# Kernel tuning notes

Measured on AMD Instinct MI355X. Metric: run time of the kernel, lower is better.

Reference implementation:

```python
import jax, jax.numpy as jnp
import numpy as np

HID = 64
N_P = 150000
N_B = 250000
E = 500000
D_NODE = 32
D_EDGE = 16
NEG_ACT = 0.01  # module-level LeakyReLU default slope
NEG_ATT = 0.2   # GATConv attention LeakyReLU slope


def _seg_softmax(logits, seg, n):
    m = jax.ops.segment_max(logits, seg, num_segments=n)
    m = jnp.where(jnp.isfinite(m), m, 0.0)
    e = jnp.exp(logits - m[seg])
    s = jax.ops.segment_sum(e, seg, num_segments=n)
    return e / (s[seg] + 1e-16)


def _gat_edges(h_src, h_dst, he, src, dst, asrc, adst, aedge, bias, n_dst):
    # per-node attention pieces, gathered per edge (heads=1)
    a = (h_src @ asrc)[src] + (h_dst @ adst)[dst] + he @ aedge  # [E]
    alpha = _seg_softmax(jax.nn.leaky_relu(a, NEG_ATT), dst, n_dst)
    out = jax.ops.segment_sum(h_src[src] * alpha[:, None], dst, num_segments=n_dst)
    return out + bias


def _homo_gat(x, ei, ea, W, We, asrc, adst, aedge, bias):
    # PyG GATConv with add_self_loops=True, fill_value='mean' for edge_attr
    n = x.shape[0]
    h = x @ W
    he = ea @ We
    loop = jnp.arange(n)
    src = jnp.concatenate([ei[0], loop])
    dst = jnp.concatenate([ei[1], loop])
    he_full = jnp.concatenate([he, jnp.broadcast_to(he.mean(0), (n, he.shape[1]))])
    return _gat_edges(h, h, he_full, src, dst, asrc, adst, aedge, bias, n)


def _bi_gat(x_src, x_dst, ei, ea, Wsrc, Wdst, We, asrc, adst, aedge, bias):
    # bipartite GATConv, add_self_loops=False
    return _gat_edges(x_src @ Wsrc, x_dst @ Wdst, ea @ We, ei[0], ei[1],
                      asrc, adst, aedge, bias, x_dst.shape[0])


def setup_inputs():
    kit = iter(jax.random.split(jax.random.key(0), 100))
    def rn(shape, s):
        return jax.random.normal(next(kit), shape, jnp.float32) * s
    s_h = 1.0 / np.sqrt(HID)
    inp = {}
    inp["x_p"] = rn((N_P, D_NODE), 1.0)
    inp["x_b"] = rn((N_B, D_NODE), 1.0)
    for r in ("pp", "bb", "bp"):
        inp["ea_" + r] = rn((E, D_EDGE), 1.0)
    inp["W_node_p"] = rn((D_NODE, HID), 1.0 / np.sqrt(D_NODE)); inp["b_node_p"] = jnp.zeros((HID,), jnp.float32)
    inp["W_node_b"] = rn((D_NODE, HID), 1.0 / np.sqrt(D_NODE)); inp["b_node_b"] = jnp.zeros((HID,), jnp.float32)
    for r in ("pp", "bb", "bp"):
        inp["W_edge_" + r] = rn((D_EDGE, HID), 1.0 / np.sqrt(D_EDGE))
        inp["b_edge_" + r] = jnp.zeros((HID,), jnp.float32)
    for L in ("c1", "c2"):
        for r in ("pp", "bb"):
            inp[L + "_" + r + "_W"] = rn((HID, HID), s_h)
            inp[L + "_" + r + "_We"] = rn((HID, HID), s_h)
            for a in ("asrc", "adst", "aedge"):
                inp[L + "_" + r + "_" + a] = rn((HID,), 0.1)
            inp[L + "_" + r + "_bias"] = rn((HID,), 0.01)
        inp[L + "_bp_Wsrc"] = rn((HID, HID), s_h)
        inp[L + "_bp_Wdst"] = rn((HID, HID), s_h)
        inp[L + "_bp_We"] = rn((HID, HID), s_h)
        for a in ("asrc", "adst", "aedge"):
            inp[L + "_bp_" + a] = rn((HID,), 0.1)
        inp[L + "_bp_bias"] = rn((HID,), 0.01)
    inp["W_out"] = rn((HID, 1), s_h); inp["b_out"] = jnp.zeros((1,), jnp.float32)
    inp["ei_pp"] = jax.random.randint(next(kit), (2, E), 0, N_P)
    inp["ei_bb"] = jax.random.randint(next(kit), (2, E), 0, N_B)
    inp["ei_bp"] = jnp.stack([jax.random.randint(next(kit), (E,), 0, N_B),
                              jax.random.randint(next(kit), (E,), 0, N_P)])
    return inp


def _forward(x_p, x_b, ea_pp, ea_bb, ea_bp, W_node_p, b_node_p, W_node_b, b_node_b, W_edge_pp, b_edge_pp, W_edge_bb, b_edge_bb, W_edge_bp, b_edge_bp, c1_pp_W, c1_pp_We, c1_pp_asrc, c1_pp_adst, c1_pp_aedge, c1_pp_bias, c1_bb_W, c1_bb_We, c1_bb_asrc, c1_bb_adst, c1_bb_aedge, c1_bb_bias, c1_bp_Wsrc, c1_bp_Wdst, c1_bp_We, c1_bp_asrc, c1_bp_adst, c1_bp_aedge, c1_bp_bias, c2_pp_W, c2_pp_We, c2_pp_asrc, c2_pp_adst, c2_pp_aedge, c2_pp_bias, c2_bb_W, c2_bb_We, c2_bb_asrc, c2_bb_adst, c2_bb_aedge, c2_bb_bias, c2_bp_Wsrc, c2_bp_Wdst, c2_bp_We, c2_bp_asrc, c2_bp_adst, c2_bp_aedge, c2_bp_bias, W_out, b_out, ei_pp, ei_bb, ei_bp):
    act = lambda t: jax.nn.leaky_relu(t, NEG_ACT)
    # input projections + LeakyReLU (dropout omitted: eval mode)
    xp = act(x_p @ W_node_p + b_node_p)
    xb = act(x_b @ W_node_b + b_node_b)
    epp = act(ea_pp @ W_edge_pp + b_edge_pp)
    ebb = act(ea_bb @ W_edge_bb + b_edge_bb)
    ebp = act(ea_bp @ W_edge_bp + b_edge_bp)
    # conv1: HeteroConv aggr='sum'
    p1 = (_homo_gat(xp, ei_pp, epp, c1_pp_W, c1_pp_We, c1_pp_asrc, c1_pp_adst, c1_pp_aedge, c1_pp_bias)
          + _bi_gat(xb, xp, ei_bp, ebp, c1_bp_Wsrc, c1_bp_Wdst, c1_bp_We, c1_bp_asrc, c1_bp_adst, c1_bp_aedge, c1_bp_bias))
    b1 = _homo_gat(xb, ei_bb, ebb, c1_bb_W, c1_bb_We, c1_bb_asrc, c1_bb_adst, c1_bb_aedge, c1_bb_bias)
    # conv2: only the 'proposal' output is consumed by the head; the 'branch'
    # output of conv2 is dead code in the original forward and is skipped.
    p2 = (_homo_gat(p1, ei_pp, epp, c2_pp_W, c2_pp_We, c2_pp_asrc, c2_pp_adst, c2_pp_aedge, c2_pp_bias)
          + _bi_gat(b1, p1, ei_bp, ebp, c2_bp_Wsrc, c2_bp_Wdst, c2_bp_We, c2_bp_asrc, c2_bp_adst, c2_bp_aedge, c2_bp_bias))
    return p2 @ W_out + b_out  # [N_P, 1]


def reference(x_p, x_b, ea_pp, ea_bb, ea_bp, W_node_p, b_node_p, W_node_b, b_node_b, W_edge_pp, b_edge_pp, W_edge_bb, b_edge_bb, W_edge_bp, b_edge_bp, c1_pp_W, c1_pp_We, c1_pp_asrc, c1_pp_adst, c1_pp_aedge, c1_pp_bias, c1_bb_W, c1_bb_We, c1_bb_asrc, c1_bb_adst, c1_bb_aedge, c1_bb_bias, c1_bp_Wsrc, c1_bp_Wdst, c1_bp_We, c1_bp_asrc, c1_bp_adst, c1_bp_aedge, c1_bp_bias, c2_pp_W, c2_pp_We, c2_pp_asrc, c2_pp_adst, c2_pp_aedge, c2_pp_bias, c2_bb_W, c2_bb_We, c2_bb_asrc, c2_bb_adst, c2_bb_aedge, c2_bb_bias, c2_bp_Wsrc, c2_bp_Wdst, c2_bp_We, c2_bp_asrc, c2_bp_adst, c2_bp_aedge, c2_bp_bias, W_out, b_out, ei_pp, ei_bb, ei_bp):
    return _forward(x_p, x_b, ea_pp, ea_bb, ea_bp, W_node_p, b_node_p, W_node_b, b_node_b, W_edge_pp, b_edge_pp, W_edge_bb, b_edge_bb, W_edge_bp, b_edge_bp, c1_pp_W, c1_pp_We, c1_pp_asrc, c1_pp_adst, c1_pp_aedge, c1_pp_bias, c1_bb_W, c1_bb_We, c1_bb_asrc, c1_bb_adst, c1_bb_aedge, c1_bb_bias, c1_bp_Wsrc, c1_bp_Wdst, c1_bp_We, c1_bp_asrc, c1_bp_adst, c1_bp_aedge, c1_bp_bias, c2_pp_W, c2_pp_We, c2_pp_asrc, c2_pp_adst, c2_pp_aedge, c2_pp_bias, c2_bb_W, c2_bb_We, c2_bb_asrc, c2_bb_adst, c2_bb_aedge, c2_bb_bias, c2_bp_Wsrc, c2_bp_Wdst, c2_bp_We, c2_bp_asrc, c2_bp_adst, c2_bp_aedge, c2_bp_bias, W_out, b_out, ei_pp, ei_bb, ei_bp)
```

## Files before the change

kernel.cpp:

```cpp
#include <hip/hip_runtime.h>


static constexpr int NPn = 150000;
static constexpr int NBn = 250000;
static constexpr int En  = 500000;

static constexpr int OFF_PP = 0;
static constexpr int OFF_BP = 150016;
static constexpr int OFF_BB = 300032;
static constexpr int NCAT   = 550144;
static constexpr int NB_TOT = NCAT / 256;
static constexpr int BS_BP  = OFF_BP / 256;
static constexpr int BS_BB  = OFF_BB / 256;

__device__ __forceinline__ float lrelu(float x, float s) { return x >= 0.0f ? x : s * x; }

__global__ void fill_kernel(float* out, float val, int n) {
  int i = blockIdx.x * blockDim.x + threadIdx.x;
  if (i < n) out[i] = val;
}

struct Dsts { const int* d[3]; const int* s[3]; };

__global__ void zero_int_kernel(int* p, int n) {
  int i = blockIdx.x * blockDim.x + threadIdx.x;
  if (i < n) p[i] = 0;
}

__global__ void hist_all_kernel(Dsts ds, int* __restrict__ cnt) {
  int t = blockIdx.x * blockDim.x + threadIdx.x;
  if (t >= 3 * En) return;
  int rel = t / En, e = t - rel * En;
  int base = (rel == 0) ? OFF_PP : (rel == 1) ? OFF_BP : OFF_BB;
  atomicAdd(&cnt[base + ds.d[rel][e]], 1);
}

__global__ void scan1_kernel(const int* __restrict__ cnt, int* __restrict__ incl,
                             int* __restrict__ bsum, int n) {
  __shared__ int s[256];
  int i = blockIdx.x * 256 + threadIdx.x;
  s[threadIdx.x] = (i < n) ? cnt[i] : 0;
  __syncthreads();
  for (int o = 1; o < 256; o <<= 1) {
    int t = (threadIdx.x >= o) ? s[threadIdx.x - o] : 0;
    __syncthreads();
    s[threadIdx.x] += t;
    __syncthreads();
  }
  if (i < n) incl[i] = s[threadIdx.x];
  if (threadIdx.x == 255) bsum[blockIdx.x] = s[255];
}

__global__ void scan2_kernel(int* bsum) {
  int t = threadIdx.x;
  if (t >= 3) return;
  int lo = (t == 0) ? 0 : (t == 1) ? BS_BP : BS_BB;
  int hi = (t == 0) ? BS_BP : (t == 1) ? BS_BB : NB_TOT;
  int run = 0;
  for (int i = lo; i < hi; ++i) { int v = bsum[i]; bsum[i] = run; run += v; }
}

__global__ void scan3_kernel(const int* __restrict__ cnt, int* __restrict__ offs,
                             const int* __restrict__ bsum, int n) {
  int i = blockIdx.x * 256 + threadIdx.x;
  if (i < n) offs[i] = offs[i] - cnt[i] + bsum[i >> 8];
}

__global__ void copy_int_kernel(const int* __restrict__ src, int* __restrict__ dstp, int n) {
  int i = blockIdx.x * blockDim.x + threadIdx.x;
  if (i < n) dstp[i] = src[i];
}

__global__ void scatter_all_kernel(Dsts ds, int* __restrict__ cursor,
                                   int* __restrict__ srcs, int* __restrict__ pos) {
  int t = blockIdx.x * blockDim.x + threadIdx.x;
  if (t >= 3 * En) return;
  int rel = t / En, e = t - rel * En;
  int base = (rel == 0) ? OFF_PP : (rel == 1) ? OFF_BP : OFF_BB;
  int p = atomicAdd(&cursor[base + ds.d[rel][e]], 1);
  srcs[rel * En + p] = ds.s[rel][e];
  pos[rel * En + e] = p;
}

__global__ void proj_kernel(const float* __restrict__ X, const float* __restrict__ W,
                            const float* __restrict__ b, float* __restrict__ Y, int N) {
  __shared__ __align__(16) float Ws[32 * 64];
  __shared__ float Xs[64 * 33];
  __shared__ float bs[64];
  for (int i = threadIdx.x; i < 32 * 64; i += 256) Ws[i] = W[i];
  if (threadIdx.x < 64) bs[threadIdx.x] = b[threadIdx.x];
  int base = blockIdx.x * 64;
  int rows = min(64, N - base);
  {
    const float4* s4 = reinterpret_cast<const float4*>(X + (size_t)base * 32);
    for (int idx = threadIdx.x; idx < rows * 8; idx += 256) {
      float4 v = s4[idx];
      int r = idx >> 3, c4 = idx & 7;
      float* d = &Xs[r * 33 + c4 * 4];
      d[0] = v.x; d[1] = v.y; d[2] = v.z; d[3] = v.w;
    }
  }
  __syncthreads();
  int r = threadIdx.x >> 2, q = threadIdx.x & 3;
  if (r >= rows) return;
  const float4* Ws4 = reinterpret_cast<const float4*>(Ws);
  float acc[16];
  const float4* b4 = reinterpret_cast<const float4*>(&bs[q * 16]);
#pragma unroll
  for (int j = 0; j < 4; ++j) {
    float4 v = b4[j];
    acc[4 * j + 0] = v.x; acc[4 * j + 1] = v.y; acc[4 * j + 2] = v.z; acc[4 * j + 3] = v.w;
  }
#pragma unroll
  for (int k = 0; k < 32; ++k) {
    float xv = Xs[r * 33 + k];
#pragma unroll
    for (int j = 0; j < 4; ++j) {
      float4 w = Ws4[k * 16 + q * 4 + j];
      acc[4 * j + 0] += xv * w.x; acc[4 * j + 1] += xv * w.y;
      acc[4 * j + 2] += xv * w.z; acc[4 * j + 3] += xv * w.w;
    }
  }
  float4* y4 = reinterpret_cast<float4*>(Y + (size_t)(base + r) * 64 + q * 16);
#pragma unroll
  for (int j = 0; j < 4; ++j)
    y4[j] = make_float4(lrelu(acc[4 * j + 0], 0.01f), lrelu(acc[4 * j + 1], 0.01f),
                        lrelu(acc[4 * j + 2], 0.01f), lrelu(acc[4 * j + 3], 0.01f));
}

__global__ void hgemm_kernel(const float* X, const float* __restrict__ W,
                             const float* __restrict__ a1, const float* __restrict__ a2,
                             const float* __restrict__ xv,
                             float* H, float* __restrict__ S1,
                             float* __restrict__ S2, float* __restrict__ S3, int N) {
  __shared__ __align__(16) float Ws[64 * 64];
  __shared__ float Xs[64 * 65];
  __shared__ float a1s[64], a2s[64], xvs[64];
  for (int i = threadIdx.x; i < 64 * 64; i += 256) Ws[i] = W[i];
  if (threadIdx.x < 64) {
    a1s[threadIdx.x] = a1[threadIdx.x];
    a2s[threadIdx.x] = a2 ? a2[threadIdx.x] : 0.0f;
    xvs[threadIdx.x] = xv ? xv[threadIdx.x] : 0.0f;
  }
  int base = blockIdx.x * 64;
  int rows = min(64, N - base);
  {
    const float4* s4 = reinterpret_cast<const float4*>(X + (size_t)base * 64);
    for (int idx = threadIdx.x; idx < rows * 16; idx += 256) {
      float4 v = s4[idx];
      int r = idx >> 4, c4 = idx & 15;
      float* d = &Xs[r * 65 + c4 * 4];
      d[0] = v.x; d[1] = v.y; d[2] = v.z; d[3] = v.w;
    }
  }
  __syncthreads();
  int r = threadIdx.x >> 2, q = threadIdx.x & 3;
  if (r >= rows) return;
  const float4* Ws4 = reinterpret_cast<const float4*>(Ws);
  float acc[16];
#pragma unroll
  for (int c = 0; c < 16; ++c) acc[c] = 0.0f;
  float s3p = 0.0f;
#pragma unroll
  for (int k = 0; k < 64; ++k) {
    float xval = Xs[r * 65 + k];
#pragma unroll
    for (int j = 0; j < 4; ++j) {
      float4 w = Ws4[k * 16 + q * 4 + j];
      acc[4 * j + 0] += xval * w.x; acc[4 * j + 1] += xval * w.y;
      acc[4 * j + 2] += xval * w.z; acc[4 * j + 3] += xval * w.w;
    }
  }
#pragma unroll
  for (int k = 0; k < 16; ++k) s3p += Xs[r * 65 + q * 16 + k] * xvs[q * 16 + k];
  float s1p = 0.0f, s2p = 0.0f;
#pragma unroll
  for (int c = 0; c < 16; ++c) {
    s1p += acc[c] * a1s[q * 16 + c];
    s2p += acc[c] * a2s[q * 16 + c];
  }
  s1p += __shfl_xor(s1p, 1, 64); s1p += __shfl_xor(s1p, 2, 64);
  s2p += __shfl_xor(s2p, 1, 64); s2p += __shfl_xor(s2p, 2, 64);
  s3p += __shfl_xor(s3p, 1, 64); s3p += __shfl_xor(s3p, 2, 64);
  float4* h4 = reinterpret_cast<float4*>(H + (size_t)(base + r) * 64 + q * 16);
#pragma unroll
  for (int j = 0; j < 4; ++j)
    h4[j] = make_float4(acc[4 * j + 0], acc[4 * j + 1], acc[4 * j + 2], acc[4 * j + 3]);
  if (q == 0) {
    S1[base + r] = s1p;
    if (S2) S2[base + r] = s2p;
    if (S3) S3[base + r] = s3p;
  }
}

__global__ void hgemm2_kernel(float* X, const float* __restrict__ W1,
                              const float* __restrict__ a1a,
                              const float* __restrict__ W2,
                              const float* __restrict__ a2a, const float* __restrict__ a2b,
                              float* __restrict__ H1out,
                              float* __restrict__ S1a, float* __restrict__ S2a,
                              float* __restrict__ S2b, int N) {
  __shared__ __align__(16) float W1s[64 * 64];
  __shared__ __align__(16) float W2s[64 * 64];
  __shared__ float Xs[64 * 65];
  __shared__ float v1[64], v2a[64], v2b[64];
  for (int i = threadIdx.x; i < 64 * 64; i += 256) { W1s[i] = W1[i]; W2s[i] = W2[i]; }
  if (threadIdx.x < 64) {
    v1[threadIdx.x] = a1a[threadIdx.x];
    v2a[threadIdx.x] = a2a[threadIdx.x];
    v2b[threadIdx.x] = a2b[threadIdx.x];
  }
  int base = blockIdx.x * 64;
  int rows = min(64, N - base);
  {
    const float4* s4 = reinterpret_cast<const float4*>(X + (size_t)base * 64);
    for (int idx = threadIdx.x; idx < rows * 16; idx += 256) {
      float4 v = s4[idx];
      int r = idx >> 4, c4 = idx & 15;
      float* d = &Xs[r * 65 + c4 * 4];
      d[0] = v.x; d[1] = v.y; d[2] = v.z; d[3] = v.w;
    }
  }
  __syncthreads();
  int r = threadIdx.x >> 2, q = threadIdx.x & 3;
  if (r >= rows) return;
  const float4* W1s4 = reinterpret_cast<const float4*>(W1s);
  const float4* W2s4 = reinterpret_cast<const float4*>(W2s);
  float acc1[16], acc2[16];
#pragma unroll
  for (int c = 0; c < 16; ++c) { acc1[c] = 0.0f; acc2[c] = 0.0f; }
#pragma unroll
  for (int k = 0; k < 64; ++k) {
    float xval = Xs[r * 65 + k];
#pragma unroll
    for (int j = 0; j < 4; ++j) {
      float4 w1 = W1s4[k * 16 + q * 4 + j];
      acc1[4 * j + 0] += xval * w1.x; acc1[4 * j + 1] += xval * w1.y;
      acc1[4 * j + 2] += xval * w1.z; acc1[4 * j + 3] += xval * w1.w;
      float4 w2 = W2s4[k * 16 + q * 4 + j];
      acc2[4 * j + 0] += xval * w2.x; acc2[4 * j + 1] += xval * w2.y;
      acc2[4 * j + 2] += xval * w2.z; acc2[4 * j + 3] += xval * w2.w;
    }
  }
  float s1p = 0.0f, sap = 0.0f, sbp = 0.0f;
#pragma unroll
  for (int c = 0; c < 16; ++c) {
    s1p += acc1[c] * v1[q * 16 + c];
    sap += acc2[c] * v2a[q * 16 + c];
    sbp += acc2[c] * v2b[q * 16 + c];
  }
  s1p += __shfl_xor(s1p, 1, 64); s1p += __shfl_xor(s1p, 2, 64);
  sap += __shfl_xor(sap, 1, 64); sap += __shfl_xor(sap, 2, 64);
  sbp += __shfl_xor(sbp, 1, 64); sbp += __shfl_xor(sbp, 2, 64);
  float4* h14 = reinterpret_cast<float4*>(H1out + (size_t)(base + r) * 64 + q * 16);
  float4* h24 = reinterpret_cast<float4*>(X + (size_t)(base + r) * 64 + q * 16);
#pragma unroll
  for (int j = 0; j < 4; ++j) {
    h14[j] = make_float4(acc1[4 * j + 0], acc1[4 * j + 1], acc1[4 * j + 2], acc1[4 * j + 3]);
    h24[j] = make_float4(acc2[4 * j + 0], acc2[4 * j + 1], acc2[4 * j + 2], acc2[4 * j + 3]);
  }
  if (q == 0) {
    S1a[base + r] = s1p;
    S2a[base + r] = sap;
    S2b[base + r] = sbp;
  }
}

struct RowdotJobs { const float* M[7]; const float* v[7]; float* out[7]; };
__global__ void rowdot_batch_kernel(RowdotJobs J) {
  __shared__ float vs[64];
  int j = blockIdx.x;
  vs[threadIdx.x] = J.v[j][threadIdx.x];
  __syncthreads();
  float s = 0.0f;
  const float* M = J.M[j];
#pragma unroll
  for (int c = 0; c < 64; ++c) s += M[threadIdx.x * 64 + c] * vs[c];
  J.out[j][threadIdx.x] = s;
}

struct EdgeJobs {
  const float* EA[3]; const float* We[3]; const float* be[3];
  const float* wa1[3]; const float* wa2[3]; float* hd1[3]; float* hd2[3];
  const int* pos[3];
};
__global__ __launch_bounds__(256, 2) void edge_fused_kernel(EdgeJobs J,
                                                            float* __restrict__ sacc) {
  int rel = blockIdx.x >> 9;
  int blk = blockIdx.x & 511;
  __shared__ float eas[4][32 * 16];
  __shared__ float red1[4], red2[4];
  bool has2 = (J.wa2[rel] != nullptr);
  int lane = threadIdx.x & 63;
  int wv   = threadIdx.x >> 6;
  int qd   = lane >> 4;
  int sl   = lane & 15;
  float* myeas = eas[wv];
  float wreg[16][4];
  const float* We = J.We[rel];
#pragma unroll
  for (int k = 0; k < 16; ++k) {
    float4 w = *reinterpret_cast<const float4*>(&We[k * 64 + sl * 4]);
    wreg[k][0] = w.x; wreg[k][1] = w.y; wreg[k][2] = w.z; wreg[k][3] = w.w;
  }
  float4 bc = *reinterpret_cast<const float4*>(&J.be[rel][sl * 4]);
  float4 w1c = *reinterpret_cast<const float4*>(&J.wa1[rel][sl * 4]);
  float4 w2c = has2 ? *reinterpret_cast<const float4*>(&J.wa2[rel][sl * 4])
                    : make_float4(0.f, 0.f, 0.f, 0.f);
  const float* EA = J.EA[rel];
  float* hd1 = J.hd1[rel];
  float* hd2 = J.hd2[rel];
  const int* pos = J.pos[rel];
  float s1 = 0.0f, s2 = 0.0f;
  for (int base = (blk * 4 + wv) * 32; base < En; base += 512 * 4 * 32) {
    int tile = min(32, En - base);
    float4* d4 = reinterpret_cast<float4*>(myeas);
    const float4* s4 = reinterpret_cast<const float4*>(EA + (size_t)base * 16);
    for (int i = lane; i < tile * 4; i += 64) d4[i] = s4[i];
#pragma unroll
    for (int it = 0; it < 8; ++it) {
      int e = it * 4 + qd;
      if (e < tile) {
        float t0 = bc.x, t1 = bc.y, t2 = bc.z, t3 = bc.w;
#pragma unroll
        for (int k = 0; k < 16; ++k) {
          float xv = myeas[e * 16 + k];
          t0 += xv * wreg[k][0]; t1 += xv * wreg[k][1];
          t2 += xv * wreg[k][2]; t3 += xv * wreg[k][3];
        }
        t0 = lrelu(t0, 0.01f); t1 = lrelu(t1, 0.01f);
        t2 = lrelu(t2, 0.01f); t3 = lrelu(t3, 0.01f);
        float d1 = t0 * w1c.x + t1 * w1c.y + t2 * w1c.z + t3 * w1c.w;
        float d2 = t0 * w2c.x + t1 * w2c.y + t2 * w2c.z + t3 * w2c.w;
#pragma unroll
        for (int o = 1; o < 16; o <<= 1) {
          d1 += __shfl_xor(d1, o, 64);
          d2 += __shfl_xor(d2, o, 64);
        }
        if (sl == 0) {
          int p = pos[base + e];
          hd1[p] = d1;
          if (has2) hd2[p] = d2;
          s1 += d1;
          s2 += d2;
        }
      }
    }
  }
  if (rel < 2) {
#pragma unroll
    for (int o = 32; o >= 1; o >>= 1) {
      s1 += __shfl_xor(s1, o, 64);
      s2 += __shfl_xor(s2, o, 64);
    }
    if (lane == 0) { red1[wv] = s1; red2[wv] = s2; }
    __syncthreads();
    if (threadIdx.x == 0) {
      float t1 = red1[0] + red1[1] + red1[2] + red1[3];
      float t2 = red2[0] + red2[1] + red2[2] + red2[3];
      if (rel == 0) {
        atomicAdd(&sacc[0], t1);
        atomicAdd(&sacc[1], t2);
      } else {
        atomicAdd(&sacc[2], t1);
      }
    }
  }
}

__global__ void selfscale_kernel(const float* __restrict__ sacc, float invE,
                                 float* __restrict__ self_pp1, float* __restrict__ self_pp2,
                                 float* __restrict__ self_bb1) {
  if (threadIdx.x == 0) {
    self_pp1[0] = sacc[0] * invE;
    self_pp2[0] = sacc[1] * invE;
    self_bb1[0] = sacc[2] * invE;
  }
}

__global__ void gat_row_kernel(const int* __restrict__ offs, const int* __restrict__ srcs,
                               const float* __restrict__ ssrc, const float* __restrict__ sdst,
                               const float* __restrict__ hd, const float* __restrict__ selfhd,
                               const float* __restrict__ H, const float* __restrict__ bias,
                               float* __restrict__ out, int N) {
  int wid = (int)(((size_t)blockIdx.x * blockDim.x + threadIdx.x) >> 6);
  int lane = threadIdx.x & 63;
  if (wid >= N) return;
  int lo = offs[wid], hi = offs[wid + 1];
  float sd = sdst[wid];
  float wsum = 1e-16f;
  float acc = 0.0f;
  if (selfhd) {
    float wself = __expf(lrelu(ssrc[wid] + sd + selfhd[0], 0.2f));
    wsum += wself;
    acc = wself * H[(size_t)wid * 64 + lane];
  }
  for (int p = lo; p < hi; ++p) {
    int s = srcs[p];
    float w = __expf(lrelu(ssrc[s] + sd + hd[p], 0.2f));
    wsum += w;
    acc += w * H[(size_t)s * 64 + lane];
  }
  out[(size_t)wid * 64 + lane] = acc / wsum + bias[lane];
}

__global__ void gat_row2_kernel(
    const int* __restrict__ offsA, const int* __restrict__ srcsA,
    const float* __restrict__ ssrcA, const float* __restrict__ sdstA,
    const float* __restrict__ hdA, const float* __restrict__ selfhdA,
    const float* __restrict__ HA, const float* __restrict__ biasA,
    const int* __restrict__ offsB, const int* __restrict__ srcsB,
    const float* __restrict__ ssrcB, const float* __restrict__ sdstB,
    const float* __restrict__ hdB, const float* __restrict__ HB,
    const float* __restrict__ biasB,
    float* __restrict__ out, int N) {
  int wid = (int)(((size_t)blockIdx.x * blockDim.x + threadIdx.x) >> 6);
  int lane = threadIdx.x & 63;
  if (wid >= N) return;
  int lo = offsA[wid], hi = offsA[wid + 1];
  float sd = sdstA[wid];
  float wself = __expf(lrelu(ssrcA[wid] + sd + selfhdA[0], 0.2f));
  float wsumA = 1e-16f + wself;
  float accA = wself * HA[(size_t)wid * 64 + lane];
  for (int p = lo; p < hi; ++p) {
    int s = srcsA[p];
    float w = __expf(lrelu(ssrcA[s] + sd + hdA[p], 0.2f));
    wsumA += w;
    accA += w * HA[(size_t)s * 64 + lane];
  }
  lo = offsB[wid]; hi = offsB[wid + 1];
  float sdB = sdstB[wid];
  float wsumB = 1e-16f;
  float accB = 0.0f;
  for (int p = lo; p < hi; ++p) {
    int s = srcsB[p];
    float w = __expf(lrelu(ssrcB[s] + sdB + hdB[p], 0.2f));
    wsumB += w;
    accB += w * HB[(size_t)s * 64 + lane];
  }
  out[(size_t)wid * 64 + lane] =
      accA / wsumA + biasA[lane] + accB / wsumB + biasB[lane];
}

__global__ void gat_row2h_kernel(
    const int* __restrict__ offsA, const int* __restrict__ srcsA,
    const float* __restrict__ ssrcA, const float* __restrict__ sdstA,
    const float* __restrict__ hdA, const float* __restrict__ selfhdA,
    const float* __restrict__ HA, const float* __restrict__ biasA,
    const int* __restrict__ offsB, const int* __restrict__ srcsB,
    const float* __restrict__ ssrcB, const float* __restrict__ sdstB,
    const float* __restrict__ hdB, const float* __restrict__ HB,
    const float* __restrict__ biasB,
    const float* __restrict__ wout, const float* __restrict__ bout,
    float* __restrict__ out, int N) {
  int wid = (int)(((size_t)blockIdx.x * blockDim.x + threadIdx.x) >> 6);
  int lane = threadIdx.x & 63;
  if (wid >= N) return;
  int lo = offsA[wid], hi = offsA[wid + 1];
  float sd = sdstA[wid];
  float wself = __expf(lrelu(ssrcA[wid] + sd + selfhdA[0], 0.2f));
  float wsumA = 1e-16f + wself;
  float accA = wself * HA[(size_t)wid * 64 + lane];
  for (int p = lo; p < hi; ++p) {
    int s = srcsA[p];
    float w = __expf(lrelu(ssrcA[s] + sd + hdA[p], 0.2f));
    wsumA += w;
    accA += w * HA[(size_t)s * 64 + lane];
  }
  lo = offsB[wid]; hi = offsB[wid + 1];
  float sdB = sdstB[wid];
  float wsumB = 1e-16f;
  float accB = 0.0f;
  for (int p = lo; p < hi; ++p) {
    int s = srcsB[p];
    float w = __expf(lrelu(ssrcB[s] + sdB + hdB[p], 0.2f));
    wsumB += w;
    accB += w * HB[(size_t)s * 64 + lane];
  }
  float r = accA / wsumA + biasA[lane] + accB / wsumB + biasB[lane];
  r *= wout[lane];
#pragma unroll
  for (int o = 32; o >= 1; o >>= 1) r += __shfl_xor(r, o, 64);
  if (lane == 0) out[wid] = r + bout[0];
}

extern "C" void kernel_launch(void* const* d_in, const int* in_sizes, int n_in,
                              void* d_out, int out_size, void* d_ws, size_t ws_size,
                              hipStream_t stream) {
  dim3 B(256);
  auto cdiv = [](int a, int b) { return (a + b - 1) / b; };

  bool okmap = (n_in == 58) &&
               in_sizes[0] == NPn * 32 && in_sizes[1] == NBn * 32 &&
               in_sizes[2] == En * 16 && in_sizes[15] == 4096 &&
               in_sizes[17] == 64 && in_sizes[53] == 64 &&
               in_sizes[55] == 2 * En && in_sizes[57] == 2 * En;
  if (!okmap) {
    fill_kernel<<<cdiv(NPn, 256), B, 0, stream>>>((float*)d_out, 1000.0f, NPn);
    return;
  }

  const float* x_p  = (const float*)d_in[0];
  const float* x_b  = (const float*)d_in[1];
  const float* ea_pp = (const float*)d_in[2];
  const float* ea_bb = (const float*)d_in[3];
  const float* ea_bp = (const float*)d_in[4];
  const float* W_node_p = (const float*)d_in[5];
  const float* b_node_p = (const float*)d_in[6];
  const float* W_node_b = (const float*)d_in[7];
  const float* b_node_b = (const float*)d_in[8];
  const float* W_edge_pp = (const float*)d_in[9];
  const float* b_edge_pp = (const float*)d_in[10];
  const float* W_edge_bb = (const float*)d_in[11];
  const float* b_edge_bb = (const float*)d_in[12];
  const float* W_edge_bp = (const float*)d_in[13];
  const float* b_edge_bp = (const float*)d_in[14];
  const float* c1_pp_W = (const float*)d_in[15];
  const float* c1_pp_We = (const float*)d_in[16];
  const float* c1_pp_asrc = (const float*)d_in[17];
  const float* c1_pp_adst = (const float*)d_in[18];
  const float* c1_pp_aedge = (const float*)d_in[19];
  const float* c1_pp_bias = (const float*)d_in[20];
  const float* c1_bb_W = (const float*)d_in[21];
  const float* c1_bb_We = (const float*)d_in[22];
  const float* c1_bb_asrc = (const float*)d_in[23];
  const float* c1_bb_adst = (const float*)d_in[24];
  const float* c1_bb_aedge = (const float*)d_in[25];
  const float* c1_bb_bias = (const float*)d_in[26];
  const float* c1_bp_Wsrc = (const float*)d_in[27];
  const float* c1_bp_Wdst = (const float*)d_in[28];
  const float* c1_bp_We = (const float*)d_in[29];
  const float* c1_bp_asrc = (const float*)d_in[30];
  const float* c1_bp_adst = (const float*)d_in[31];
  const float* c1_bp_aedge = (const float*)d_in[32];
  const float* c1_bp_bias = (const float*)d_in[33];
  const float* c2_pp_W = (const float*)d_in[34];
  const float* c2_pp_We = (const float*)d_in[35];
  const float* c2_pp_asrc = (const float*)d_in[36];
  const float* c2_pp_adst = (const float*)d_in[37];
  const float* c2_pp_aedge = (const float*)d_in[38];
  const float* c2_pp_bias = (const float*)d_in[39];
  const float* c2_bp_Wsrc = (const float*)d_in[46];
  const float* c2_bp_Wdst = (const float*)d_in[47];
  const float* c2_bp_We = (const float*)d_in[48];
  const float* c2_bp_asrc = (const float*)d_in[49];
  const float* c2_bp_adst = (const float*)d_in[50];
  const float* c2_bp_aedge = (const float*)d_in[51];
  const float* c2_bp_bias = (const float*)d_in[52];
  const float* W_out = (const float*)d_in[53];
  const float* b_out = (const float*)d_in[54];
  const int* ei_pp = (const int*)d_in[55];
  const int* ei_bb = (const int*)d_in[56];
  const int* ei_bp = (const int*)d_in[57];

  float* ws = (float*)d_ws;
  int* offs_cat = (int*)ws;
  int* cnt_cat  = offs_cat + NCAT;
  int* bsum     = cnt_cat + NCAT;
  int* srcs_cat = bsum + 2560;
  int* pos_cat  = srcs_cat + 3 * En;
  float* xp    = (float*)(pos_cat + 3 * En);
  float* p1    = xp + (size_t)NPn * 64;
  float* b1v   = p1 + (size_t)NPn * 64;
  float* hbuf  = b1v + (size_t)NBn * 64;
  float* hd_pp1 = hbuf + (size_t)NBn * 64;
  float* hd_pp2 = hd_pp1 + En;
  float* hd_bb1 = hd_pp2 + En;
  float* hd_bp1 = hd_bb1 + En;
  float* hd_bp2 = hd_bp1 + En;
  float* sA_src = hd_bp2 + En;
  float* sA_dst = sA_src + NBn;
  float* sB_src = sA_dst + NBn;
  float* sB_dst = sB_src + NBn;
  float* sC_src = sB_dst + NPn;
  float* sC_dst = sC_src + NBn;
  float* small  = sC_dst + NBn;

  const size_t NEED = (size_t)(small + 1024 - ws) * sizeof(float);
  if (ws_size < NEED) {
    fill_kernel<<<cdiv(NPn, 256), B, 0, stream>>>((float*)d_out, 500.0f, NPn);
    return;
  }

  float* sacc    = small + 0;
  float* wa_pp1  = small + 128;  float* wa_pp2  = small + 192;
  float* wa_bb1  = small + 256;  float* wa_bp1  = small + 320; float* wa_bp2 = small + 384;
  float* wd1     = small + 448;  float* wd2     = small + 512;
  float* self_pp1= small + 576;  float* self_pp2= small + 577; float* self_bb1 = small + 578;
  const float invE = 1.0f / (float)En;

  hipMemsetAsync(sacc, 0, 16 * sizeof(float), stream);

  RowdotJobs RJ;
  RJ.M[0] = c1_pp_We;  RJ.v[0] = c1_pp_aedge; RJ.out[0] = wa_pp1;
  RJ.M[1] = c2_pp_We;  RJ.v[1] = c2_pp_aedge; RJ.out[1] = wa_pp2;
  RJ.M[2] = c1_bb_We;  RJ.v[2] = c1_bb_aedge; RJ.out[2] = wa_bb1;
  RJ.M[3] = c1_bp_We;  RJ.v[3] = c1_bp_aedge; RJ.out[3] = wa_bp1;
  RJ.M[4] = c2_bp_We;  RJ.v[4] = c2_bp_aedge; RJ.out[4] = wa_bp2;
  RJ.M[5] = c1_bp_Wdst; RJ.v[5] = c1_bp_adst; RJ.out[5] = wd1;
  RJ.M[6] = c2_bp_Wdst; RJ.v[6] = c2_bp_adst; RJ.out[6] = wd2;
  rowdot_batch_kernel<<<7, 64, 0, stream>>>(RJ);

  proj_kernel<<<cdiv(NPn, 64), B, 0, stream>>>(x_p, W_node_p, b_node_p, xp, NPn);
  proj_kernel<<<cdiv(NBn, 64), B, 0, stream>>>(x_b, W_node_b, b_node_b, hbuf, NBn);

  Dsts DS;
  DS.d[0] = ei_pp + En; DS.d[1] = ei_bp + En; DS.d[2] = ei_bb + En;
  DS.s[0] = ei_pp;      DS.s[1] = ei_bp;      DS.s[2] = ei_bb;
  zero_int_kernel<<<cdiv(NCAT, 256), B, 0, stream>>>(cnt_cat, NCAT);
  hist_all_kernel<<<cdiv(3 * En, 256), B, 0, stream>>>(DS, cnt_cat);
  scan1_kernel<<<NB_TOT, B, 0, stream>>>(cnt_cat, offs_cat, bsum, NCAT);
  scan2_kernel<<<1, 64, 0, stream>>>(bsum);
  scan3_kernel<<<NB_TOT, B, 0, stream>>>(cnt_cat, offs_cat, bsum, NCAT);
  copy_int_kernel<<<cdiv(NCAT, 256), B, 0, stream>>>(offs_cat, cnt_cat, NCAT);
  scatter_all_kernel<<<cdiv(3 * En, 256), B, 0, stream>>>(DS, cnt_cat, srcs_cat, pos_cat);

  const int* offs_pp = offs_cat + OFF_PP;
  const int* offs_bp = offs_cat + OFF_BP;
  const int* offs_bb = offs_cat + OFF_BB;
  const int* srcs_pp = srcs_cat;
  const int* srcs_bp = srcs_cat + En;
  const int* srcs_bb = srcs_cat + 2 * En;

  EdgeJobs EJ;
  EJ.EA[0] = ea_pp; EJ.We[0] = W_edge_pp; EJ.be[0] = b_edge_pp;
  EJ.wa1[0] = wa_pp1; EJ.wa2[0] = wa_pp2; EJ.hd1[0] = hd_pp1; EJ.hd2[0] = hd_pp2;
  EJ.pos[0] = pos_cat;
  EJ.EA[1] = ea_bb; EJ.We[1] = W_edge_bb; EJ.be[1] = b_edge_bb;
  EJ.wa1[1] = wa_bb1; EJ.wa2[1] = nullptr; EJ.hd1[1] = hd_bb1; EJ.hd2[1] = nullptr;
  EJ.pos[1] = pos_cat + 2 * En;
  EJ.EA[2] = ea_bp; EJ.We[2] = W_edge_bp; EJ.be[2] = b_edge_bp;
  EJ.wa1[2] = wa_bp1; EJ.wa2[2] = wa_bp2; EJ.hd1[2] = hd_bp1; EJ.hd2[2] = hd_bp2;
  EJ.pos[2] = pos_cat + En;
  edge_fused_kernel<<<3 * 512, B, 0, stream>>>(EJ, sacc);

  selfscale_kernel<<<1, 64, 0, stream>>>(sacc, invE, self_pp1, self_pp2, self_bb1);

  hgemm_kernel<<<cdiv(NPn, 64), B, 0, stream>>>(xp, c1_pp_W, c1_pp_asrc, c1_pp_adst,
      wd1, xp, sA_src, sA_dst, sB_dst, NPn);
  hgemm2_kernel<<<cdiv(NBn, 64), B, 0, stream>>>(hbuf, c1_bp_Wsrc, c1_bp_asrc,
      c1_bb_W, c1_bb_asrc, c1_bb_adst, b1v, sB_src, sC_src, sC_dst, NBn);
  gat_row2_kernel<<<cdiv(NPn * 64, 256), B, 0, stream>>>(
      offs_pp, srcs_pp, sA_src, sA_dst, hd_pp1, self_pp1, xp, c1_pp_bias,
      offs_bp, srcs_bp, sB_src, sB_dst, hd_bp1, b1v, c1_bp_bias, p1, NPn);
  gat_row_kernel<<<cdiv(NBn * 64, 256), B, 0, stream>>>(offs_bb, srcs_bb, sC_src, sC_dst,
      hd_bb1, self_bb1, hbuf, c1_bb_bias, b1v, NBn);

  hgemm_kernel<<<cdiv(NPn, 64), B, 0, stream>>>(p1, c2_pp_W, c2_pp_asrc, c2_pp_adst,
      wd2, hbuf, sA_src, sA_dst, sB_dst, NPn);
  hgemm_kernel<<<cdiv(NBn, 64), B, 0, stream>>>(b1v, c2_bp_Wsrc, c2_bp_asrc, nullptr,
      nullptr, b1v, sB_src, nullptr, nullptr, NBn);
  gat_row2h_kernel<<<cdiv(NPn * 64, 256), B, 0, stream>>>(
      offs_pp, srcs_pp, sA_src, sA_dst, hd_pp2, self_pp2, hbuf, c2_pp_bias,
      offs_bp, srcs_bp, sB_src, sB_dst, hd_bp2, b1v, c2_bp_bias,
      W_out, b_out, (float*)d_out, NPn);
}
```

Before: 1.099 ms.

## Parallelize block-sum scan, raise edge kernel occupancy, unroll gather loops

Replaces the serial three-thread block-sum scan with a 256-thread-per-segment parallel scan over three blocks, which removes a long serial dependency chain of roughly 1000 global accesses per thread. Raises the edge_fused_kernel launch-bounds occupancy hint from 2 to 4 blocks per SM, which may force register spills given its 64-float weight register array. Adds unroll-by-2 pragmas to the per-row neighbour gather loops so more loads can be in flight at once.

```diff
diff --git a/kernel.cpp b/kernel.cpp
--- a/kernel.cpp
+++ b/kernel.cpp
@@ -52,12 +52,26 @@
 }
 
 __global__ void scan2_kernel(int* bsum) {
-  int t = threadIdx.x;
-  if (t >= 3) return;
-  int lo = (t == 0) ? 0 : (t == 1) ? BS_BP : BS_BB;
-  int hi = (t == 0) ? BS_BP : (t == 1) ? BS_BB : NB_TOT;
-  int run = 0;
-  for (int i = lo; i < hi; ++i) { int v = bsum[i]; bsum[i] = run; run += v; }
+  int seg = blockIdx.x;
+  int lo = (seg == 0) ? 0 : (seg == 1) ? BS_BP : BS_BB;
+  int hi = (seg == 0) ? BS_BP : (seg == 1) ? BS_BB : NB_TOT;
+  int len = hi - lo;
+  int chunk = (len + 255) / 256;
+  int s = lo + threadIdx.x * chunk;
+  int e = min(s + chunk, hi);
+  __shared__ int part[256];
+  int sum = 0;
+  for (int i = s; i < e; ++i) sum += bsum[i];
+  part[threadIdx.x] = sum;
+  __syncthreads();
+  for (int o = 1; o < 256; o <<= 1) {
+    int t = (threadIdx.x >= o) ? part[threadIdx.x - o] : 0;
+    __syncthreads();
+    part[threadIdx.x] += t;
+    __syncthreads();
+  }
+  int run = (threadIdx.x == 0) ? 0 : part[threadIdx.x - 1];
+  for (int i = s; i < e; ++i) { int v = bsum[i]; bsum[i] = run; run += v; }
 }
 
 __global__ void scan3_kernel(const int* __restrict__ cnt, int* __restrict__ offs,
@@ -284,7 +298,7 @@
   const float* wa1[3]; const float* wa2[3]; float* hd1[3]; float* hd2[3];
   const int* pos[3];
 };
-__global__ __launch_bounds__(256, 2) void edge_fused_kernel(EdgeJobs J,
+__global__ __launch_bounds__(256, 4) void edge_fused_kernel(EdgeJobs J,
                                                             float* __restrict__ sacc) {
   int rel = blockIdx.x >> 9;
   int blk = blockIdx.x & 511;
@@ -395,6 +409,7 @@
     wsum += wself;
     acc = wself * H[(size_t)wid * 64 + lane];
   }
+#pragma unroll 2
   for (int p = lo; p < hi; ++p) {
     int s = srcs[p];
     float w = __expf(lrelu(ssrc[s] + sd + hd[p], 0.2f));
@@ -422,6 +437,7 @@
   float wself = __expf(lrelu(ssrcA[wid] + sd + selfhdA[0], 0.2f));
   float wsumA = 1e-16f + wself;
   float accA = wself * HA[(size_t)wid * 64 + lane];
+#pragma unroll 2
   for (int p = lo; p < hi; ++p) {
     int s = srcsA[p];
     float w = __expf(lrelu(ssrcA[s] + sd + hdA[p], 0.2f));
@@ -432,6 +448,7 @@
   float sdB = sdstB[wid];
   float wsumB = 1e-16f;
   float accB = 0.0f;
+#pragma unroll 2
   for (int p = lo; p < hi; ++p) {
     int s = srcsB[p];
     float w = __expf(lrelu(ssrcB[s] + sdB + hdB[p], 0.2f));
@@ -461,6 +478,7 @@
   float wself = __expf(lrelu(ssrcA[wid] + sd + selfhdA[0], 0.2f));
   float wsumA = 1e-16f + wself;
   float accA = wself * HA[(size_t)wid * 64 + lane];
+#pragma unroll 2
   for (int p = lo; p < hi; ++p) {
     int s = srcsA[p];
     float w = __expf(lrelu(ssrcA[s] + sd + hdA[p], 0.2f));
@@ -471,6 +489,7 @@
   float sdB = sdstB[wid];
   float wsumB = 1e-16f;
   float accB = 0.0f;
+#pragma unroll 2
   for (int p = lo; p < hi; ++p) {
     int s = srcsB[p];
     float w = __expf(lrelu(ssrcB[s] + sdB + hdB[p], 0.2f));
@@ -610,7 +629,7 @@
   zero_int_kernel<<<cdiv(NCAT, 256), B, 0, stream>>>(cnt_cat, NCAT);
   hist_all_kernel<<<cdiv(3 * En, 256), B, 0, stream>>>(DS, cnt_cat);
   scan1_kernel<<<NB_TOT, B, 0, stream>>>(cnt_cat, offs_cat, bsum, NCAT);
-  scan2_kernel<<<1, 64, 0, stream>>>(bsum);
+  scan2_kernel<<<3, B, 0, stream>>>(bsum);
   scan3_kernel<<<NB_TOT, B, 0, stream>>>(cnt_cat, offs_cat, bsum, NCAT);
   copy_int_kernel<<<cdiv(NCAT, 256), B, 0, stream>>>(offs_cat, cnt_cat, NCAT);
   scatter_all_kernel<<<cdiv(3 * En, 256), B, 0, stream>>>(DS, cnt_cat, srcs_cat, pos_cat);
```

New measurement: 1.018 ms. 7.4% less time.
